# Kernel optimization log

Measured on AMD Instinct MI355X. Metric: run time of the kernel, lower is better.

## Reference

```python
import jax, jax.numpy as jnp
import numpy as np


def setup_inputs() -> dict:
    key = jax.random.key(0)
    k1, k2, k3 = jax.random.split(key, 3)
    B, S, E = 4, 4096, 512
    x = jax.random.normal(k1, (B, S, E), dtype=jnp.float32)
    # xavier_uniform for Linear weights; zero biases (per _reset_parameters)
    lim_qkv = float(np.sqrt(6.0 / (E + 3 * E)))
    W_qkv = jax.random.uniform(k2, (3 * E, E), minval=-lim_qkv, maxval=lim_qkv, dtype=jnp.float32)
    b_qkv = jnp.zeros((3 * E,), dtype=jnp.float32)
    lim_out = float(np.sqrt(6.0 / (E + E)))
    W_out = jax.random.uniform(k3, (E, E), minval=-lim_out, maxval=lim_out, dtype=jnp.float32)
    b_out = jnp.zeros((E,), dtype=jnp.float32)
    return {"x": x, "W_qkv": W_qkv, "b_qkv": b_qkv, "W_out": W_out, "b_out": b_out}


def reference(x, W_qkv, b_qkv, W_out, b_out):
    B, S, E = x.shape
    H = 8
    D = E // H
    qkv = x @ W_qkv.T + b_qkv                      # [B,S,3E]
    qkv = qkv.reshape(B, S, H, 3 * D)
    q, k, v = jnp.split(qkv, 3, axis=-1)            # each [B,S,H,D]
    q = jax.nn.sigmoid(q)
    k = jax.nn.sigmoid(k)
    # flow conservation normalizers (sum over seq dim=1, then feature dim=3)
    i = jnp.sum(q * jnp.sum(k, axis=1, keepdims=True), axis=3, keepdims=True)      # [B,S,H,1]
    o = jnp.sum(k * jnp.sum(q, axis=1, keepdims=True), axis=3, keepdims=True)
    i_hat = jnp.sum(q * jnp.sum(k / o, axis=1, keepdims=True), axis=3, keepdims=True)
    o_hat = jnp.sum(k * jnp.sum(q / i, axis=1, keepdims=True), axis=3, keepdims=True)
    # NOTE: faithful to source — matmul batches over (B,S) and contracts the HEAD axis
    vw = v * jax.nn.softmax(o_hat, axis=1)          # [B,S,H,D]
    kv = jnp.einsum('bshd,bshe->bsde', k, vw)       # [B,S,D,D]
    r = jnp.einsum('bshd,bsde->bshe', q / i, kv) * jax.nn.sigmoid(i_hat)  # [B,S,H,D]
    values = r.reshape(B, S, E)
    return values @ W_out.T + b_out
```

## Files before the change

### kernel.cpp

```cpp
#include <hip/hip_runtime.h>
#include <cstdint>
#include <cstddef>

#define B_ 4
#define S_ 4096
#define E_ 512
#define NPOS 16384
#define QKVC 1536
#define K_ 512

typedef unsigned short u16;
typedef u16    u16x8  __attribute__((ext_vector_type(8)));
typedef u16    u16x4  __attribute__((ext_vector_type(4)));
typedef __bf16 bf16x8 __attribute__((ext_vector_type(8)));
typedef float  f32x4  __attribute__((ext_vector_type(4)));

__device__ __forceinline__ u16 f2bf(float f) {
    unsigned u = __builtin_bit_cast(unsigned, f);
    unsigned r = (u + 0x7fffu + ((u >> 16) & 1u)) >> 16;
    return (u16)r;
}
__device__ __forceinline__ float bf2f(u16 u) {
    return __builtin_bit_cast(float, (unsigned)u << 16);
}
__device__ __forceinline__ float rcpf(float x) { return __builtin_amdgcn_rcpf(x); }

__device__ __forceinline__ void async16(const void* g, void* lds) {
    __builtin_amdgcn_global_load_lds(
        (const __attribute__((address_space(1))) unsigned int*)g,
        (__attribute__((address_space(3))) unsigned int*)lds, 16, 0, 0);
}

__global__ void cvt_kernel(const float4* __restrict__ in, u16x4* __restrict__ out, int n4) {
    int i = blockIdx.x * 256 + threadIdx.x;
    if (i < n4) {
        float4 v = in[i];
        u16x4 o;
        o[0] = f2bf(v.x); o[1] = f2bf(v.y); o[2] = f2bf(v.z); o[3] = f2bf(v.w);
        out[i] = o;
    }
}

__global__ __launch_bounds__(512) void gemm_qkv(
        const u16* __restrict__ A, const u16* __restrict__ Bw,
        const float* __restrict__ bias,
        u16* __restrict__ Qb, u16* __restrict__ Kb, u16* __restrict__ Vb,
        float* __restrict__ sumq, float* __restrict__ sumk,
        int K) {
    __shared__ u16 As[4][256 * 32];
    __shared__ u16 Bs[4][256 * 32];
    const int tid  = threadIdx.x;
    const int wave = tid >> 6, lane = tid & 63;
    const int m0 = blockIdx.y * 256, n0 = blockIdx.x * 256;
    const int wm = (wave >> 2) * 128;
    const int wn = (wave & 3) * 64;

    const int srow = tid >> 2;
    const int scol = (tid & 3) * 8;
    const u16* Ap = A  + (size_t)(m0 + srow) * K + scol;
    const u16* Bp = Bw + (size_t)(n0 + srow) * K + scol;
    const int woff = wave * 512;
    const size_t rstep = (size_t)128 * K;

    f32x4 acc[8][4] = {};
    const int fr = lane & 15, fk = (lane >> 4) * 8;

    #define STAGE(t)                                                     \
        { int bb = (t) & 3;                                              \
          async16(Ap + (t) * 32,         &As[bb][woff]);                 \
          async16(Ap + (t) * 32 + rstep, &As[bb][woff + 4096]);          \
          async16(Bp + (t) * 32,         &Bs[bb][woff]);                 \
          async16(Bp + (t) * 32 + rstep, &Bs[bb][woff + 4096]); }

    const int NT = K >> 5;
    STAGE(0); STAGE(1); STAGE(2);
    asm volatile("s_waitcnt vmcnt(8)" ::: "memory");
    __builtin_amdgcn_s_barrier();
    __builtin_amdgcn_sched_barrier(0);

    for (int t = 0; t < NT; ++t) {
        const u16* Ab = As[t & 3];
        const u16* Bb = Bs[t & 3];
        if (t + 3 < NT) STAGE(t + 3);
        bf16x8 b[4], a[8];
        #pragma unroll
        for (int j = 0; j < 4; ++j)
            b[j] = *(const bf16x8*)&Bb[(wn + j * 16 + fr) * 32 + fk];
        #pragma unroll
        for (int i = 0; i < 8; ++i)
            a[i] = *(const bf16x8*)&Ab[(wm + i * 16 + fr) * 32 + fk];
        __builtin_amdgcn_s_setprio(1);
        #pragma unroll
        for (int i = 0; i < 8; ++i)
            #pragma unroll
            for (int j = 0; j < 4; ++j)
                acc[i][j] = __builtin_amdgcn_mfma_f32_16x16x32_bf16(a[i], b[j], acc[i][j], 0, 0, 0);
        __builtin_amdgcn_s_setprio(0);
        if (t < NT - 1) {
            if (t < NT - 3)       asm volatile("s_waitcnt vmcnt(8)" ::: "memory");
            else if (t == NT - 3) asm volatile("s_waitcnt vmcnt(4)" ::: "memory");
            else                  asm volatile("s_waitcnt vmcnt(0)" ::: "memory");
            __builtin_amdgcn_s_barrier();
            __builtin_amdgcn_sched_barrier(0);
        }
    }
    #undef STAGE

    const int cn = lane & 15, rb = (lane >> 4) * 4;
    const int cg   = (n0 + wn) >> 6;
    const int type = cg % 3;
    const int hb   = cg / 3;
    u16* dst = (type == 0) ? Qb : (type == 1) ? Kb : Vb;
    const bool sg = (type < 2);
    float colsum[4] = {};
    #pragma unroll
    for (int i = 0; i < 8; ++i) {
        int mbase = m0 + wm + i * 16 + rb;
        #pragma unroll
        for (int j = 0; j < 4; ++j) {
            int ccol = j * 16 + cn;
            float bv = bias[n0 + wn + ccol];
            int outcol = hb * 64 + ccol;
            f32x4 av = acc[i][j];
            #pragma unroll
            for (int r = 0; r < 4; ++r) {
                float v = av[r] + bv;
                if (sg) { v = 1.f / (1.f + __expf(-v)); colsum[j] += v; }
                dst[(size_t)(mbase + r) * 512 + outcol] = f2bf(v);
            }
        }
    }
    if (sg) {
        float* sdst = (type == 0) ? sumq : sumk;
        const int b = m0 >> 12;
        #pragma unroll
        for (int j = 0; j < 4; ++j) {
            float s = colsum[j];
            s += __shfl_xor(s, 16);
            s += __shfl_xor(s, 32);
            if (lane < 16)
                atomicAdd(&sdst[b * 512 + hb * 64 + j * 16 + cn], s);
        }
    }
}

__device__ __forceinline__ void mfma_step(const u16* AsB, const u16* BsB,
                                          int wm, int wn, int fr, int fkk,
                                          f32x4 (&acc)[4][4]) {
    bf16x8 a[4], b[4];
    #pragma unroll
    for (int i = 0; i < 4; ++i)
        a[i] = *(const bf16x8*)&AsB[(wm + i * 16 + fr) * 32 + fkk];
    #pragma unroll
    for (int j = 0; j < 4; ++j)
        b[j] = *(const bf16x8*)&BsB[(wn + j * 16 + fr) * 32 + fkk];
    __builtin_amdgcn_s_setprio(1);
    #pragma unroll
    for (int i = 0; i < 4; ++i)
        #pragma unroll
        for (int j = 0; j < 4; ++j)
            acc[i][j] = __builtin_amdgcn_mfma_f32_16x16x32_bf16(a[i], b[j], acc[i][j], 0, 0, 0);
    __builtin_amdgcn_s_setprio(0);
}

__global__ __launch_bounds__(256) void gemm_out(
        const u16* __restrict__ A, const u16* __restrict__ Bw,
        const float* __restrict__ bias, float* __restrict__ C,
        int N, int K) {
    __shared__ u16 As[3][128 * 32];
    __shared__ u16 Bs[3][128 * 32];
    const int tid  = threadIdx.x;
    const int wave = tid >> 6, lane = tid & 63;
    const int m0 = blockIdx.y * 128, n0 = blockIdx.x * 128;
    const int wm = (wave & 1) * 64, wn = (wave >> 1) * 64;
    const int srow = wave * 16 + (lane >> 2);
    const int cgs  = (lane & 3) ^ ((lane >> 2) & 3) ^ ((lane >> 4) & 3);
    const u16* Ap = A  + (size_t)(m0 + srow) * K + cgs * 8;
    const u16* Bp = Bw + (size_t)(n0 + srow) * K + cgs * 8;
    const int woff = wave * 512;
    const size_t rstep = (size_t)64 * K;
    f32x4 acc[4][4] = {};
    const int fr  = lane & 15;
    const int fkk = (((lane >> 4) ^ (fr & 3) ^ ((fr >> 2) & 3))) * 8;

    #define STAGE(t, buf)                                             \
        async16(Ap + (t) * 32,         &As[buf][woff]);               \
        async16(Ap + (t) * 32 + rstep, &As[buf][woff + 2048]);        \
        async16(Bp + (t) * 32,         &Bs[buf][woff]);               \
        async16(Bp + (t) * 32 + rstep, &Bs[buf][woff + 2048]);

    const int nt = K >> 5;
    STAGE(0, 0);
    STAGE(1, 1);
    asm volatile("s_waitcnt vmcnt(4)" ::: "memory");
    __builtin_amdgcn_s_barrier();
    __builtin_amdgcn_sched_barrier(0);
    int cb = 0, sb = 1;
    for (int t = 0; t < nt - 2; ++t) {
        sb = (sb == 2) ? 0 : sb + 1;
        STAGE(t + 2, sb);
        mfma_step(As[cb], Bs[cb], wm, wn, fr, fkk, acc);
        asm volatile("s_waitcnt vmcnt(4)" ::: "memory");
        __builtin_amdgcn_s_barrier();
        __builtin_amdgcn_sched_barrier(0);
        cb = (cb == 2) ? 0 : cb + 1;
    }
    mfma_step(As[cb], Bs[cb], wm, wn, fr, fkk, acc);
    asm volatile("s_waitcnt vmcnt(0)" ::: "memory");
    __builtin_amdgcn_s_barrier();
    __builtin_amdgcn_sched_barrier(0);
    cb = (cb == 2) ? 0 : cb + 1;
    mfma_step(As[cb], Bs[cb], wm, wn, fr, fkk, acc);
    #undef STAGE

    const int cn = lane & 15, rb = (lane >> 4) * 4;
    #pragma unroll
    for (int i = 0; i < 4; ++i) {
        int mbase = m0 + wm + i * 16 + rb;
        #pragma unroll
        for (int j = 0; j < 4; ++j) {
            int nn = n0 + wn + j * 16 + cn;
            float bv = bias[nn];
            f32x4 av = acc[i][j];
            #pragma unroll
            for (int r = 0; r < 4; ++r)
                C[(size_t)(mbase + r) * N + nn] = av[r] + bv;
        }
    }
}

__global__ __launch_bounds__(256) void fused_io(const u16* __restrict__ Qg, const u16* __restrict__ Kg,
                                                const float* __restrict__ sumq, const float* __restrict__ sumk,
                                                float* __restrict__ iv,
                                                float* __restrict__ sumqi, float* __restrict__ sumko) {
    int b = blockIdx.x, sc = blockIdx.y;
    int w = threadIdx.x >> 6, lane = threadIdx.x & 63;
    float skL[8], sqL[8];
    #pragma unroll
    for (int j = 0; j < 8; ++j) {
        skL[j] = sumk[b * 512 + lane * 8 + j];
        sqL[j] = sumq[b * 512 + lane * 8 + j];
    }
    float aqi[8] = {}, ako[8] = {};
    int p0 = b * S_ + sc * 32 + w * 8;
    for (int it = 0; it < 8; ++it) {
        int p = p0 + it;
        size_t off = (size_t)p * 512 + lane * 8;
        u16x8 q8 = *(const u16x8*)(Qg + off);
        u16x8 k8 = *(const u16x8*)(Kg + off);
        float qf[8], kf[8];
        #pragma unroll
        for (int j = 0; j < 8; ++j) { qf[j] = bf2f(q8[j]); kf[j] = bf2f(k8[j]); }
        float di = 0.f, dox = 0.f;
        #pragma unroll
        for (int j = 0; j < 8; ++j) { di += qf[j] * skL[j]; dox += kf[j] * sqL[j]; }
        di  += __shfl_xor(di, 1);  di  += __shfl_xor(di, 2);  di  += __shfl_xor(di, 4);
        dox += __shfl_xor(dox, 1); dox += __shfl_xor(dox, 2); dox += __shfl_xor(dox, 4);
        if ((lane & 7) == 0) iv[(size_t)p * 8 + (lane >> 3)] = di;
        float ri = rcpf(di), ro = rcpf(dox);
        #pragma unroll
        for (int j = 0; j < 8; ++j) { aqi[j] += qf[j] * ri; ako[j] += kf[j] * ro; }
    }
    __shared__ float red[4][1024];
    #pragma unroll
    for (int j = 0; j < 8; ++j) {
        red[w][lane * 8 + j]       = aqi[j];
        red[w][512 + lane * 8 + j] = ako[j];
    }
    __syncthreads();
    int t = threadIdx.x;
    #pragma unroll
    for (int rr = 0; rr < 4; ++rr) {
        int slot = rr * 256 + t;
        float s = red[0][slot] + red[1][slot] + red[2][slot] + red[3][slot];
        float* dst = (slot < 512) ? &sumqi[b * 512 + slot] : &sumko[b * 512 + (slot - 512)];
        atomicAdd(dst, s);
    }
}

__global__ __launch_bounds__(256) void io2_kernel(const u16* __restrict__ Qg, const u16* __restrict__ Kg,
                                                  const float* __restrict__ sumqi, const float* __restrict__ sumko,
                                                  const float* __restrict__ iv,
                                                  float* __restrict__ rowsc, float* __restrict__ wexp,
                                                  float* __restrict__ sm) {
    int b = blockIdx.x, sc = blockIdx.y;
    int w = threadIdx.x >> 6, lane = threadIdx.x & 63;
    float skoL[8], sqiL[8];
    #pragma unroll
    for (int j = 0; j < 8; ++j) {
        skoL[j] = sumko[b * 512 + lane * 8 + j];
        sqiL[j] = sumqi[b * 512 + lane * 8 + j];
    }
    float smacc = 0.f;
    int p0 = b * S_ + sc * 32 + w * 8;
    for (int it = 0; it < 8; ++it) {
        int p = p0 + it;
        size_t off = (size_t)p * 512 + lane * 8;
        u16x8 q8 = *(const u16x8*)(Qg + off);
        u16x8 k8 = *(const u16x8*)(Kg + off);
        float dih = 0.f, doh = 0.f;
        #pragma unroll
        for (int j = 0; j < 8; ++j) {
            dih += bf2f(q8[j]) * skoL[j];
            doh += bf2f(k8[j]) * sqiL[j];
        }
        dih += __shfl_xor(dih, 1); dih += __shfl_xor(dih, 2); dih += __shfl_xor(dih, 4);
        doh += __shfl_xor(doh, 1); doh += __shfl_xor(doh, 2); doh += __shfl_xor(doh, 4);
        if ((lane & 7) == 0) {
            int h = lane >> 3;
            float sig = 1.f / (1.f + __expf(-dih));
            rowsc[(size_t)p * 8 + h] = sig * rcpf(iv[(size_t)p * 8 + h]);
            float we = __expf(fminf(doh, 80.f));
            wexp[(size_t)p * 8 + h] = we;
            smacc += we;
        }
    }
    __shared__ float sr[4][8];
    if ((lane & 7) == 0) sr[w][lane >> 3] = smacc;
    __syncthreads();
    if (threadIdx.x < 8)
        atomicAdd(&sm[b * 8 + threadIdx.x],
                  sr[0][threadIdx.x] + sr[1][threadIdx.x] + sr[2][threadIdx.x] + sr[3][threadIdx.x]);
}

__global__ __launch_bounds__(256) void finalize_kernel(
        const u16* __restrict__ Qg, const u16* __restrict__ Kg, const u16* __restrict__ Vg,
        const float* __restrict__ rowsc, const float* __restrict__ wexp, const float* __restrict__ sm,
        u16* __restrict__ Rg) {
    __shared__ float Ml[4][2][8][9];
    __shared__ float vw[4][2][8][68];
    int w = threadIdx.x >> 6, lane = threadIdx.x & 63;
    int p0 = (blockIdx.x * 4 + w) * 2;
    int b = p0 >> 12;

    {
        int pl = (lane >> 3) & 1, hh = lane & 7, quad = lane >> 4;
        const u16* qa = Qg + (size_t)(p0 + pl) * 512 + hh * 64 + quad * 8;
        const u16* ka = Kg + (size_t)(p0 + pl) * 512 + hh * 64 + quad * 8;
        bf16x8 a0 = __builtin_bit_cast(bf16x8, *(const u16x8*)qa);
        bf16x8 a1 = __builtin_bit_cast(bf16x8, *(const u16x8*)(qa + 32));
        bf16x8 b0 = __builtin_bit_cast(bf16x8, *(const u16x8*)ka);
        bf16x8 b1 = __builtin_bit_cast(bf16x8, *(const u16x8*)(ka + 32));
        f32x4 accm = {0.f, 0.f, 0.f, 0.f};
        accm = __builtin_amdgcn_mfma_f32_16x16x32_bf16(a0, b0, accm, 0, 0, 0);
        accm = __builtin_amdgcn_mfma_f32_16x16x32_bf16(a1, b1, accm, 0, 0, 0);
        if (((lane >> 5) & 1) == ((lane >> 3) & 1)) {
            int plm = lane >> 5, hr = ((lane >> 4) & 1) * 4, h2 = lane & 7;
            #pragma unroll
            for (int r = 0; r < 4; ++r) Ml[w][plm][hr + r][h2] = accm[r];
        }
    }
    {
        int hv = lane >> 3, e0 = (lane & 7) * 8;
        float invsm = rcpf(sm[b * 8 + hv]);
        #pragma unroll
        for (int pl = 0; pl < 2; ++pl) {
            u16x8 v8 = *(const u16x8*)(Vg + (size_t)(p0 + pl) * 512 + lane * 8);
            float wgt = wexp[(size_t)(p0 + pl) * 8 + hv] * invsm;
            f32x4 x0, x1;
            #pragma unroll
            for (int j = 0; j < 4; ++j) { x0[j] = bf2f(v8[j]) * wgt; x1[j] = bf2f(v8[4 + j]) * wgt; }
            *(f32x4*)&vw[w][pl][hv][e0]     = x0;
            *(f32x4*)&vw[w][pl][hv][e0 + 4] = x1;
        }
    }
    __syncthreads();
    {
        int pl = lane >> 5, idx = lane & 31, h = idx >> 2, eq = (idx & 3) * 16;
        float out[16] = {};
        #pragma unroll
        for (int h2 = 0; h2 < 8; ++h2) {
            float m = Ml[w][pl][h][h2];
            #pragma unroll
            for (int c = 0; c < 4; ++c) {
                f32x4 vv = *(const f32x4*)&vw[w][pl][h2][eq + c * 4];
                #pragma unroll
                for (int j = 0; j < 4; ++j) out[c * 4 + j] += m * vv[j];
            }
        }
        float rs = rowsc[(size_t)(p0 + pl) * 8 + h];
        u16x8 o0, o1;
        #pragma unroll
        for (int j = 0; j < 8; ++j) { o0[j] = f2bf(out[j] * rs); o1[j] = f2bf(out[8 + j] * rs); }
        u16* dst = Rg + (size_t)(p0 + pl) * 512 + h * 64 + eq;
        *(u16x8*)dst       = o0;
        *(u16x8*)(dst + 8) = o1;
    }
}

extern "C" void kernel_launch(void* const* d_in, const int* in_sizes, int n_in,
                              void* d_out, int out_size, void* d_ws, size_t ws_size,
                              hipStream_t stream) {
    const float* x    = (const float*)d_in[0];
    const float* Wqkv = (const float*)d_in[1];
    const float* bqkv = (const float*)d_in[2];
    const float* Wout = (const float*)d_in[3];
    const float* bout = (const float*)d_in[4];
    float* out = (float*)d_out;
    char* ws = (char*)d_ws;

    constexpr size_t SZ_XBF  = (size_t)NPOS * E_ * 2;
    constexpr size_t SZ_WQBF = (size_t)QKVC * E_ * 2;
    constexpr size_t SZ_WOBF = (size_t)E_ * E_ * 2;
    constexpr size_t SZ_QKVB = (size_t)NPOS * E_ * 2;
    constexpr size_t SZ_SUM  = (size_t)B_ * 512 * 4;
    constexpr size_t SZ_V8   = (size_t)NPOS * 8 * 4;

    size_t off = 0;
    u16*   xbf   = (u16*)(ws + off);   off += SZ_XBF;
    u16*   wqbf  = (u16*)(ws + off);   off += SZ_WQBF;
    u16*   wobf  = (u16*)(ws + off);   off += SZ_WOBF;
    u16*   Qb    = (u16*)(ws + off);   off += SZ_QKVB;
    u16*   Kb    = (u16*)(ws + off);   off += SZ_QKVB;
    u16*   Vb    = (u16*)(ws + off);   off += SZ_QKVB;
    char*  zbase = ws + off;
    float* sumq  = (float*)(ws + off); off += SZ_SUM;
    float* sumk  = (float*)(ws + off); off += SZ_SUM;
    float* sumqi = (float*)(ws + off); off += SZ_SUM;
    float* sumko = (float*)(ws + off); off += SZ_SUM;
    float* sm    = (float*)(ws + off); off += 256;
    size_t zlen  = (char*)(ws + off) - zbase;
    float* iv    = (float*)(ws + off); off += SZ_V8;
    float* rowsc = (float*)(ws + off); off += SZ_V8;
    float* wexp  = (float*)(ws + off); off += SZ_V8;
    u16*   rbf   = xbf;

    hipMemsetAsync(zbase, 0, zlen, stream);

    cvt_kernel<<<(NPOS * E_ / 4) / 256, 256, 0, stream>>>((const float4*)x, (u16x4*)xbf, NPOS * E_ / 4);
    cvt_kernel<<<(QKVC * E_ / 4) / 256, 256, 0, stream>>>((const float4*)Wqkv, (u16x4*)wqbf, QKVC * E_ / 4);
    cvt_kernel<<<(E_ * E_ / 4) / 256, 256, 0, stream>>>((const float4*)Wout, (u16x4*)wobf, E_ * E_ / 4);

    gemm_qkv<<<dim3(QKVC / 256, NPOS / 256), 512, 0, stream>>>(xbf, wqbf, bqkv, Qb, Kb, Vb, sumq, sumk, K_);

    fused_io<<<dim3(B_, 128), 256, 0, stream>>>(Qb, Kb, sumq, sumk, iv, sumqi, sumko);
    io2_kernel<<<dim3(B_, 128), 256, 0, stream>>>(Qb, Kb, sumqi, sumko, iv, rowsc, wexp, sm);
    finalize_kernel<<<NPOS / 8, 256, 0, stream>>>(Qb, Kb, Vb, rowsc, wexp, sm, rbf);

    gemm_out<<<dim3(E_ / 128, NPOS / 128), 256, 0, stream>>>(rbf, wobf, bout, out, E_, K_);
}
```

Measured before the change: 210.4 us.

## Fuse conversion kernels, retile QKV GEMM, swizzle block order in both GEMMs

Merges the three fp32-to-bf16 conversion launches into one kernel. Changes the QKV GEMM from 256x256 tiles with 8 waves and a 4-stage pipeline to 256x128 tiles with 4 waves and a 3-stage pipeline. Both GEMMs switch to a 1D grid with an XCD-aware block swizzle meant to improve L2 locality. The XOR LDS swizzle in gemm_out is removed, which may bring back LDS bank conflicts. The goals are fewer launches, better occupancy and better cache reuse, at the cost of less operand reuse per block in the QKV GEMM.

After: 214.9 us. 2.2% more time.

```diff
diff --git a/kernel.cpp b/kernel.cpp
--- a/kernel.cpp
+++ b/kernel.cpp
@@ -31,85 +31,100 @@
         (__attribute__((address_space(3))) unsigned int*)lds, 16, 0, 0);
 }
 
-__global__ void cvt_kernel(const float4* __restrict__ in, u16x4* __restrict__ out, int n4) {
+#define CVT_N1 (NPOS * E_ / 4)
+#define CVT_N2 (QKVC * E_ / 4)
+#define CVT_N3 (E_ * E_ / 4)
+__global__ void cvt_all(const float4* __restrict__ x,  u16x4* __restrict__ xo,
+                        const float4* __restrict__ wq, u16x4* __restrict__ wqo,
+                        const float4* __restrict__ wo, u16x4* __restrict__ woo) {
     int i = blockIdx.x * 256 + threadIdx.x;
-    if (i < n4) {
-        float4 v = in[i];
-        u16x4 o;
-        o[0] = f2bf(v.x); o[1] = f2bf(v.y); o[2] = f2bf(v.z); o[3] = f2bf(v.w);
-        out[i] = o;
-    }
-}
-
-__global__ __launch_bounds__(512) void gemm_qkv(
+    const float4* in; u16x4* out; int idx;
+    if (i < CVT_N1)                { in = x;  out = xo;  idx = i; }
+    else if (i < CVT_N1 + CVT_N2)  { in = wq; out = wqo; idx = i - CVT_N1; }
+    else                           { in = wo; out = woo; idx = i - CVT_N1 - CVT_N2; }
+    float4 v = in[idx];
+    u16x4 o;
+    o[0] = f2bf(v.x); o[1] = f2bf(v.y); o[2] = f2bf(v.z); o[3] = f2bf(v.w);
+    out[idx] = o;
+}
+
+__global__ __launch_bounds__(256) void gemm_qkv(
         const u16* __restrict__ A, const u16* __restrict__ Bw,
         const float* __restrict__ bias,
         u16* __restrict__ Qb, u16* __restrict__ Kb, u16* __restrict__ Vb,
         float* __restrict__ sumq, float* __restrict__ sumk,
         int K) {
-    __shared__ u16 As[4][256 * 32];
-    __shared__ u16 Bs[4][256 * 32];
+    __shared__ u16 As[3][256 * 32];
+    __shared__ u16 Bs[3][128 * 32];
     const int tid  = threadIdx.x;
     const int wave = tid >> 6, lane = tid & 63;
-    const int m0 = blockIdx.y * 256, n0 = blockIdx.x * 256;
-    const int wm = (wave >> 2) * 128;
-    const int wn = (wave & 3) * 64;
+    const int bid = blockIdx.x;
+    const int swz = (bid & 7) * 96 + (bid >> 3);
+    const int m0 = (swz / 12) * 256, n0 = (swz % 12) * 128;
+    const int wm = (wave & 1) * 128, wn = (wave >> 1) * 64;
 
     const int srow = tid >> 2;
     const int scol = (tid & 3) * 8;
     const u16* Ap = A  + (size_t)(m0 + srow) * K + scol;
     const u16* Bp = Bw + (size_t)(n0 + srow) * K + scol;
-    const int woff = wave * 512;
-    const size_t rstep = (size_t)128 * K;
+    const size_t rstep = (size_t)64 * K;
 
     f32x4 acc[8][4] = {};
     const int fr = lane & 15, fk = (lane >> 4) * 8;
 
-    #define STAGE(t)                                                     \
-        { int bb = (t) & 3;                                              \
-          async16(Ap + (t) * 32,         &As[bb][woff]);                 \
-          async16(Ap + (t) * 32 + rstep, &As[bb][woff + 4096]);          \
-          async16(Bp + (t) * 32,         &Bs[bb][woff]);                 \
-          async16(Bp + (t) * 32 + rstep, &Bs[bb][woff + 4096]); }
-
-    const int NT = K >> 5;
-    STAGE(0); STAGE(1); STAGE(2);
-    asm volatile("s_waitcnt vmcnt(8)" ::: "memory");
+    #define STAGEQ(t, bb)                                                  \
+        { async16(Ap + (t) * 32,             &As[bb][tid * 8]);            \
+          async16(Ap + (t) * 32 + rstep,     &As[bb][tid * 8 + 2048]);     \
+          async16(Ap + (t) * 32 + 2 * rstep, &As[bb][tid * 8 + 4096]);     \
+          async16(Ap + (t) * 32 + 3 * rstep, &As[bb][tid * 8 + 6144]);     \
+          async16(Bp + (t) * 32,             &Bs[bb][tid * 8]);            \
+          async16(Bp + (t) * 32 + rstep,     &Bs[bb][tid * 8 + 2048]); }
+
+    #define MFMAQ(cb)                                                      \
+        { bf16x8 a[8], b[4];                                               \
+          _Pragma("unroll")                                                \
+          for (int j = 0; j < 4; ++j)                                      \
+              b[j] = *(const bf16x8*)&Bs[cb][(wn + j * 16 + fr) * 32 + fk];\
+          _Pragma("unroll")                                                \
+          for (int i = 0; i < 8; ++i)                                      \
+              a[i] = *(const bf16x8*)&As[cb][(wm + i * 16 + fr) * 32 + fk];\
+          __builtin_amdgcn_s_setprio(1);                                   \
+          _Pragma("unroll")                                                \
+          for (int i = 0; i < 8; ++i)                                      \
+              _Pragma("unroll")                                            \
+              for (int j = 0; j < 4; ++j)                                  \
+                  acc[i][j] = __builtin_amdgcn_mfma_f32_16x16x32_bf16(a[i], b[j], acc[i][j], 0, 0, 0); \
+          __builtin_amdgcn_s_setprio(0); }
+
+    const int nt = K >> 5;
+    STAGEQ(0, 0)
+    STAGEQ(1, 1)
+    asm volatile("s_waitcnt vmcnt(6)" ::: "memory");
     __builtin_amdgcn_s_barrier();
     __builtin_amdgcn_sched_barrier(0);
-
-    for (int t = 0; t < NT; ++t) {
-        const u16* Ab = As[t & 3];
-        const u16* Bb = Bs[t & 3];
-        if (t + 3 < NT) STAGE(t + 3);
-        bf16x8 b[4], a[8];
-        #pragma unroll
-        for (int j = 0; j < 4; ++j)
-            b[j] = *(const bf16x8*)&Bb[(wn + j * 16 + fr) * 32 + fk];
-        #pragma unroll
-        for (int i = 0; i < 8; ++i)
-            a[i] = *(const bf16x8*)&Ab[(wm + i * 16 + fr) * 32 + fk];
-        __builtin_amdgcn_s_setprio(1);
-        #pragma unroll
-        for (int i = 0; i < 8; ++i)
-            #pragma unroll
-            for (int j = 0; j < 4; ++j)
-                acc[i][j] = __builtin_amdgcn_mfma_f32_16x16x32_bf16(a[i], b[j], acc[i][j], 0, 0, 0);
-        __builtin_amdgcn_s_setprio(0);
-        if (t < NT - 1) {
-            if (t < NT - 3)       asm volatile("s_waitcnt vmcnt(8)" ::: "memory");
-            else if (t == NT - 3) asm volatile("s_waitcnt vmcnt(4)" ::: "memory");
-            else                  asm volatile("s_waitcnt vmcnt(0)" ::: "memory");
-            __builtin_amdgcn_s_barrier();
-            __builtin_amdgcn_sched_barrier(0);
-        }
-    }
-    #undef STAGE
+    int cb = 0, sb = 1;
+    for (int t = 0; t < nt - 2; ++t) {
+        sb = (sb == 2) ? 0 : sb + 1;
+        STAGEQ(t + 2, sb)
+        MFMAQ(cb)
+        asm volatile("s_waitcnt vmcnt(6)" ::: "memory");
+        __builtin_amdgcn_s_barrier();
+        __builtin_amdgcn_sched_barrier(0);
+        cb = (cb == 2) ? 0 : cb + 1;
+    }
+    MFMAQ(cb)
+    asm volatile("s_waitcnt vmcnt(0)" ::: "memory");
+    __builtin_amdgcn_s_barrier();
+    __builtin_amdgcn_sched_barrier(0);
+    cb = (cb == 2) ? 0 : cb + 1;
+    MFMAQ(cb)
+    #undef STAGEQ
+    #undef MFMAQ
 
     const int cn = lane & 15, rb = (lane >> 4) * 4;
-    const int cg   = (n0 + wn) >> 6;
-    const int type = cg % 3;
-    const int hb   = cg / 3;
+    const int cg2  = (n0 + wn) >> 6;
+    const int type = cg2 % 3;
+    const int hb   = cg2 / 3;
     u16* dst = (type == 0) ? Qb : (type == 1) ? Kb : Vb;
     const bool sg = (type < 2);
     float colsum[4] = {};
@@ -171,17 +186,19 @@
     __shared__ u16 Bs[3][128 * 32];
     const int tid  = threadIdx.x;
     const int wave = tid >> 6, lane = tid & 63;
-    const int m0 = blockIdx.y * 128, n0 = blockIdx.x * 128;
+    const int bid = blockIdx.x;
+    const int swz = (bid & 7) * 64 + (bid >> 3);
+    const int m0 = (swz >> 2) * 128, n0 = (swz & 3) * 128;
     const int wm = (wave & 1) * 64, wn = (wave >> 1) * 64;
     const int srow = wave * 16 + (lane >> 2);
-    const int cgs  = (lane & 3) ^ ((lane >> 2) & 3) ^ ((lane >> 4) & 3);
-    const u16* Ap = A  + (size_t)(m0 + srow) * K + cgs * 8;
-    const u16* Bp = Bw + (size_t)(n0 + srow) * K + cgs * 8;
+    const int scol = (lane & 3) * 8;
+    const u16* Ap = A  + (size_t)(m0 + srow) * K + scol;
+    const u16* Bp = Bw + (size_t)(n0 + srow) * K + scol;
     const int woff = wave * 512;
     const size_t rstep = (size_t)64 * K;
     f32x4 acc[4][4] = {};
     const int fr  = lane & 15;
-    const int fkk = (((lane >> 4) ^ (fr & 3) ^ ((fr >> 2) & 3))) * 8;
+    const int fkk = (lane >> 4) * 8;
 
     #define STAGE(t, buf)                                             \
         async16(Ap + (t) * 32,         &As[buf][woff]);               \
@@ -427,15 +444,16 @@
 
     hipMemsetAsync(zbase, 0, zlen, stream);
 
-    cvt_kernel<<<(NPOS * E_ / 4) / 256, 256, 0, stream>>>((const float4*)x, (u16x4*)xbf, NPOS * E_ / 4);
-    cvt_kernel<<<(QKVC * E_ / 4) / 256, 256, 0, stream>>>((const float4*)Wqkv, (u16x4*)wqbf, QKVC * E_ / 4);
-    cvt_kernel<<<(E_ * E_ / 4) / 256, 256, 0, stream>>>((const float4*)Wout, (u16x4*)wobf, E_ * E_ / 4);
-
-    gemm_qkv<<<dim3(QKVC / 256, NPOS / 256), 512, 0, stream>>>(xbf, wqbf, bqkv, Qb, Kb, Vb, sumq, sumk, K_);
+    cvt_all<<<(CVT_N1 + CVT_N2 + CVT_N3) / 256, 256, 0, stream>>>(
+        (const float4*)x, (u16x4*)xbf,
+        (const float4*)Wqkv, (u16x4*)wqbf,
+        (const float4*)Wout, (u16x4*)wobf);
+
+    gemm_qkv<<<dim3((QKVC / 128) * (NPOS / 256)), 256, 0, stream>>>(xbf, wqbf, bqkv, Qb, Kb, Vb, sumq, sumk, K_);
 
     fused_io<<<dim3(B_, 128), 256, 0, stream>>>(Qb, Kb, sumq, sumk, iv, sumqi, sumko);
     io2_kernel<<<dim3(B_, 128), 256, 0, stream>>>(Qb, Kb, sumqi, sumko, iv, rowsc, wexp, sm);
     finalize_kernel<<<NPOS / 8, 256, 0, stream>>>(Qb, Kb, Vb, rowsc, wexp, sm, rbf);
 
-    gemm_out<<<dim3(E_ / 128, NPOS / 128), 256, 0, stream>>>(rbf, wobf, bout, out, E_, K_);
-}
+    gemm_out<<<dim3((E_ / 128) * (NPOS / 128)), 256, 0, stream>>>(rbf, wobf, bout, out, E_, K_);
+}
```
